# Performance work log

Hardware: AMD Instinct MI355X
Metric: run time of the kernel (lower is better)

The kernel has to match this reference:

```python
import jax, jax.numpy as jnp
import numpy as np

DIM = 1024
B, SQ, SK = 8, 2048, 2048


def setup_inputs() -> dict:
    key = jax.random.key(0)
    ks = jax.random.split(key, 8)
    s = 1.0 / np.sqrt(DIM)
    return {
        "x": jax.random.normal(ks[0], (B, SQ, DIM), dtype=jnp.float32),
        "context": jax.random.normal(ks[1], (B, SK, DIM), dtype=jnp.float32),
        "Wq": jax.random.normal(ks[2], (DIM, DIM), dtype=jnp.float32) * s,
        "bq": jnp.zeros((DIM,), dtype=jnp.float32),
        "Wk": jax.random.normal(ks[3], (DIM, DIM), dtype=jnp.float32) * s,
        "bk": jnp.zeros((DIM,), dtype=jnp.float32),
        "Wv": jax.random.normal(ks[4], (DIM, DIM), dtype=jnp.float32) * s,
        "bv": jnp.zeros((DIM,), dtype=jnp.float32),
    }


def reference(x, context, Wq, bq, Wk, bk, Wv, bv):
    # nn.Linear: y = x @ W.T + b
    q = jnp.einsum("bsd,ed->bse", x, Wq) + bq          # [B, SQ, D]
    k = jnp.einsum("btd,ed->bte", context, Wk) + bk    # [B, SK, D]
    v = jnp.einsum("btd,ed->bte", context, Wv) + bv    # [B, SK, D]
    scale = 1.0 / jnp.sqrt(jnp.asarray(x.shape[-1], dtype=x.dtype))
    scores = jnp.einsum("bse,bte->bst", q, k) * scale  # [B, SQ, SK]
    attn = jax.nn.softmax(scores, axis=-1)
    return jnp.einsum("bst,bte->bse", attn, v)         # [B, SQ, D]
```

## Files before the change

### kernel.cpp

```cpp
#include <hip/hip_runtime.h>
#include <hip/hip_bf16.h>
#include <hip/hip_fp16.h>

typedef float f32x4 __attribute__((ext_vector_type(4)));
typedef short short8 __attribute__((ext_vector_type(8)));
typedef _Float16 h4 __attribute__((ext_vector_type(4)));
typedef unsigned short u16;
typedef unsigned int u32;

#define LDK 40

__device__ __forceinline__ u16 bf16_rne(float x) {
  u32 u = __float_as_uint(x);
  u += 0x7FFFu + ((u >> 16) & 1u);
  return (u16)(u >> 16);
}
__device__ __forceinline__ u32 pack2(float a, float b) {
  return (u32)bf16_rne(a) | ((u32)bf16_rne(b) << 16);
}

__global__ __launch_bounds__(256)
void convert_kernel(const float* __restrict__ x, const float* __restrict__ ctx,
                    const float* __restrict__ wq, const float* __restrict__ wk,
                    const float* __restrict__ wv,
                    u16* __restrict__ xb, u16* __restrict__ cb,
                    u16* __restrict__ wqb, u16* __restrict__ wkb,
                    u16* __restrict__ wvb)
{
  int blk = blockIdx.x;
  const float* src; u16* dst; size_t off;
  if (blk < 8192)       { src = x;   dst = xb;  off = (size_t)blk * 2048; }
  else if (blk < 16384) { src = ctx; dst = cb;  off = (size_t)(blk - 8192) * 2048; }
  else if (blk < 16896) { src = wq;  dst = wqb; off = (size_t)(blk - 16384) * 2048; }
  else if (blk < 17408) { src = wk;  dst = wkb; off = (size_t)(blk - 16896) * 2048; }
  else                  { src = wv;  dst = wvb; off = (size_t)(blk - 17408) * 2048; }
  size_t e = off + (size_t)threadIdx.x * 8;
  float4 a = *(const float4*)(src + e);
  float4 b = *(const float4*)(src + e + 4);
  uint4 o;
  o.x = pack2(a.x, a.y); o.y = pack2(a.z, a.w);
  o.z = pack2(b.x, b.y); o.w = pack2(b.z, b.w);
  *(uint4*)(dst + e) = o;
}

__device__ __forceinline__ void stage_tile(const u16* __restrict__ G, int ld,
                                           int kt, u16* L, int tid) {
#pragma unroll
  for (int it = 0; it < 2; ++it) {
    int s = tid + 256 * it;
    int r = s >> 2, c = s & 3;
    *(uint4*)&L[r * LDK + c * 8] = *(const uint4*)(G + (size_t)r * ld + kt + c * 8);
  }
}

#define GEMM_FRAGS_AND_MFMA(Ah, Bh)                                            \
  short8 a_f[4], b_f[4];                                                       \
  _Pragma("unroll")                                                            \
  for (int i = 0; i < 4; ++i) {                                                \
    a_f[i] = *(const short8*)&Ah[(wm + i * 16 + lrow) * LDK + quad * 8];       \
    b_f[i] = *(const short8*)&Bh[(wn + i * 16 + lrow) * LDK + quad * 8];       \
  }                                                                            \
  _Pragma("unroll")                                                            \
  for (int i = 0; i < 4; ++i)                                                  \
    _Pragma("unroll")                                                          \
    for (int j = 0; j < 4; ++j)                                                \
      acc[i][j] = __builtin_amdgcn_mfma_f32_16x16x32_bf16(a_f[i], b_f[j], acc[i][j], 0, 0, 0);

#define GEMM_PROLOGUE                                                          \
  const int tid = threadIdx.x;                                                 \
  const int w = tid >> 6, lane = tid & 63;                                     \
  const int wm = (w >> 1) * 64, wn = (w & 1) * 64;                             \
  const int lrow = lane & 15, quad = lane >> 4;                                \
  f32x4 acc[4][4];                                                             \
  _Pragma("unroll")                                                            \
  for (int i = 0; i < 4; ++i)                                                  \
    _Pragma("unroll")                                                          \
    for (int j = 0; j < 4; ++j) {                                              \
      f32x4 z = {0.f, 0.f, 0.f, 0.f};                                          \
      acc[i][j] = z;                                                           \
    }

__global__ __launch_bounds__(256)
void projq_kernel(const u16* __restrict__ A, const u16* __restrict__ W,
                  const float* __restrict__ bias, u16* __restrict__ Y)
{
  __shared__ __align__(16) u16 Ah[128 * LDK];
  __shared__ __align__(16) u16 Bh[128 * LDK];
  const int m0 = blockIdx.y * 128, n0 = blockIdx.x * 128;
  GEMM_PROLOGUE
  const u16* A_b = A + (size_t)m0 * 1024;
  const u16* B_b = W + (size_t)n0 * 1024;

  for (int kt = 0; kt < 1024; kt += 32) {
    __syncthreads();
    stage_tile(A_b, 1024, kt, Ah, tid);
    stage_tile(B_b, 1024, kt, Bh, tid);
    __syncthreads();
    GEMM_FRAGS_AND_MFMA(Ah, Bh)
  }

#pragma unroll
  for (int j = 0; j < 4; ++j) {
    int gn = n0 + wn + j * 16 + lrow;
    float bj = bias[gn];
#pragma unroll
    for (int i = 0; i < 4; ++i) {
      int gm_base = m0 + wm + i * 16 + quad * 4;
#pragma unroll
      for (int r = 0; r < 4; ++r)
        Y[(size_t)(gm_base + r) * 1024 + gn] = bf16_rne(acc[i][j][r] + bj);
    }
  }
}

__global__ __launch_bounds__(256)
void projv_kernel(const u16* __restrict__ A, const u16* __restrict__ W,
                  const float* __restrict__ bias, u16* __restrict__ Vt)
{
  __shared__ __align__(16) u16 smem[128 * 136];
  u16* Ah = smem;
  u16* Bh = smem + 128 * LDK;
  const int m0 = blockIdx.y * 128, n0 = blockIdx.x * 128;
  const int bb = m0 >> 11, t0 = m0 & 2047;
  GEMM_PROLOGUE
  const u16* A_b = A + (size_t)m0 * 1024;
  const u16* B_b = W + (size_t)n0 * 1024;

  for (int kt = 0; kt < 1024; kt += 32) {
    __syncthreads();
    stage_tile(A_b, 1024, kt, Ah, tid);
    stage_tile(B_b, 1024, kt, Bh, tid);
    __syncthreads();
    GEMM_FRAGS_AND_MFMA(Ah, Bh)
  }

  __syncthreads();
  u16* T = smem;
#pragma unroll
  for (int j = 0; j < 4; ++j) {
    int e_l = wn + j * 16 + lrow;
    float bj = bias[n0 + e_l];
#pragma unroll
    for (int i = 0; i < 4; ++i) {
      int t_l = wm + i * 16 + quad * 4;
      uint2 p;
      p.x = pack2(acc[i][j][0] + bj, acc[i][j][1] + bj);
      p.y = pack2(acc[i][j][2] + bj, acc[i][j][3] + bj);
      *(uint2*)&T[e_l * 136 + t_l] = p;
    }
  }
  __syncthreads();

  int e_l = tid >> 1, half = tid & 1;
  u16* gdst = Vt + ((size_t)(bb * 1024 + n0 + e_l)) * 2048 + t0 + half * 64;
  const u16* Trow = &T[e_l * 136 + half * 64];
#pragma unroll
  for (int k = 0; k < 8; ++k)
    *(uint4*)(gdst + k * 8) = *(const uint4*)(Trow + k * 8);
}

__global__ __launch_bounds__(256)
void score_kernel(const u16* __restrict__ qb, const u16* __restrict__ kb,
                  _Float16* __restrict__ S)
{
  __shared__ __align__(16) u16 Ah[128 * LDK];
  __shared__ __align__(16) u16 Bh[128 * LDK];
  const int b = blockIdx.z;
  const int m0 = blockIdx.y * 128, n0 = blockIdx.x * 128;
  GEMM_PROLOGUE
  const u16* A_b = qb + ((size_t)b * 2048 + m0) * 1024;
  const u16* B_b = kb + ((size_t)b * 2048 + n0) * 1024;

  for (int kt = 0; kt < 1024; kt += 32) {
    __syncthreads();
    stage_tile(A_b, 1024, kt, Ah, tid);
    stage_tile(B_b, 1024, kt, Bh, tid);
    __syncthreads();
    GEMM_FRAGS_AND_MFMA(Ah, Bh)
  }

  const float scale = 0.03125f;
#pragma unroll
  for (int j = 0; j < 4; ++j) {
    int gn = n0 + wn + j * 16 + lrow;
#pragma unroll
    for (int i = 0; i < 4; ++i) {
      int gm_base = m0 + wm + i * 16 + quad * 4;
#pragma unroll
      for (int r = 0; r < 4; ++r)
        S[((size_t)b * 2048 + gm_base + r) * 2048 + gn] = (_Float16)(acc[i][j][r] * scale);
    }
  }
}

__global__ __launch_bounds__(256)
void softmax_kernel(_Float16* __restrict__ S)
{
  const int row = blockIdx.x;
  const int tid = threadIdx.x;
  _Float16* Sr = S + (size_t)row * 2048;
  h4 ah = *(const h4*)(Sr + tid * 4);
  h4 bh = *(const h4*)(Sr + 1024 + tid * 4);
  float a0 = (float)ah.x, a1 = (float)ah.y, a2 = (float)ah.z, a3 = (float)ah.w;
  float b0 = (float)bh.x, b1 = (float)bh.y, b2 = (float)bh.z, b3 = (float)bh.w;

  float m = fmaxf(fmaxf(fmaxf(a0, a1), fmaxf(a2, a3)),
                  fmaxf(fmaxf(b0, b1), fmaxf(b2, b3)));
#pragma unroll
  for (int off = 32; off > 0; off >>= 1) m = fmaxf(m, __shfl_xor(m, off));

  __shared__ float red[4];
  const int wid = tid >> 6, lane = tid & 63;
  if (lane == 0) red[wid] = m;
  __syncthreads();
  m = fmaxf(fmaxf(red[0], red[1]), fmaxf(red[2], red[3]));

  float e0 = __expf(a0 - m), e1 = __expf(a1 - m), e2 = __expf(a2 - m), e3 = __expf(a3 - m);
  float e4 = __expf(b0 - m), e5 = __expf(b1 - m), e6 = __expf(b2 - m), e7 = __expf(b3 - m);
  float s = ((e0 + e1) + (e2 + e3)) + ((e4 + e5) + (e6 + e7));
#pragma unroll
  for (int off = 32; off > 0; off >>= 1) s += __shfl_xor(s, off);
  __syncthreads();
  if (lane == 0) red[wid] = s;
  __syncthreads();
  s = red[0] + red[1] + red[2] + red[3];
  float inv = 1.0f / s;

  u16* P = (u16*)S;
  size_t pb = (size_t)row * 2048;
  uint2 w0, w1;
  w0.x = pack2(e0 * inv, e1 * inv);
  w0.y = pack2(e2 * inv, e3 * inv);
  w1.x = pack2(e4 * inv, e5 * inv);
  w1.y = pack2(e6 * inv, e7 * inv);
  *(uint2*)&P[pb + tid * 4] = w0;
  *(uint2*)&P[pb + 1024 + tid * 4] = w1;
}

__global__ __launch_bounds__(256)
void pv_kernel(const u16* __restrict__ P, const u16* __restrict__ Vt,
               float* __restrict__ O)
{
  __shared__ __align__(16) u16 Ah[128 * LDK];
  __shared__ __align__(16) u16 Bh[128 * LDK];
  const int b = blockIdx.z;
  const int m0 = blockIdx.y * 128, n0 = blockIdx.x * 128;
  GEMM_PROLOGUE
  const u16* A_b = P + ((size_t)b * 2048 + m0) * 2048;
  const u16* B_b = Vt + ((size_t)b * 1024 + n0) * 2048;

  for (int kt = 0; kt < 2048; kt += 32) {
    __syncthreads();
    stage_tile(A_b, 2048, kt, Ah, tid);
    stage_tile(B_b, 2048, kt, Bh, tid);
    __syncthreads();
    GEMM_FRAGS_AND_MFMA(Ah, Bh)
  }

#pragma unroll
  for (int j = 0; j < 4; ++j) {
    int gn = n0 + wn + j * 16 + lrow;
#pragma unroll
    for (int i = 0; i < 4; ++i) {
      int gm_base = m0 + wm + i * 16 + quad * 4;
#pragma unroll
      for (int r = 0; r < 4; ++r)
        O[((size_t)b * 2048 + gm_base + r) * 1024 + gn] = acc[i][j][r];
    }
  }
}

extern "C" void kernel_launch(void* const* d_in, const int* in_sizes, int n_in,
                              void* d_out, int out_size, void* d_ws, size_t ws_size,
                              hipStream_t stream) {
  const float* x   = (const float*)d_in[0];
  const float* ctx = (const float*)d_in[1];
  const float* Wq  = (const float*)d_in[2];
  const float* bq  = (const float*)d_in[3];
  const float* Wk  = (const float*)d_in[4];
  const float* bk  = (const float*)d_in[5];
  const float* Wv  = (const float*)d_in[6];
  const float* bv  = (const float*)d_in[7];
  float* out = (float*)d_out;

  const size_t NQ = (size_t)16384 * 1024;
  const size_t NW = (size_t)1024 * 1024;
  const size_t needed = (5 * NQ + 3 * NW) * sizeof(u16);
  if (ws_size < needed) return;

  u16* xb  = (u16*)d_ws;
  u16* cb  = xb + NQ;
  u16* qb  = cb + NQ;
  u16* kb  = qb + NQ;
  u16* vt  = kb + NQ;
  u16* wqb = vt + NQ;
  u16* wkb = wqb + NW;
  u16* wvb = wkb + NW;
  _Float16* S = (_Float16*)d_ws;

  dim3 blk(256, 1, 1);
  hipLaunchKernelGGL(convert_kernel, dim3(17920, 1, 1), blk, 0, stream,
                     x, ctx, Wq, Wk, Wv, xb, cb, wqb, wkb, wvb);
  hipLaunchKernelGGL(projq_kernel, dim3(8, 128, 1), blk, 0, stream, xb, wqb, bq, qb);
  hipLaunchKernelGGL(projq_kernel, dim3(8, 128, 1), blk, 0, stream, cb, wkb, bk, kb);
  hipLaunchKernelGGL(projv_kernel, dim3(8, 128, 1), blk, 0, stream, cb, wvb, bv, vt);
  hipLaunchKernelGGL(score_kernel, dim3(16, 16, 8), blk, 0, stream, qb, kb, S);
  hipLaunchKernelGGL(softmax_kernel, dim3(16384, 1, 1), blk, 0, stream, S);
  hipLaunchKernelGGL(pv_kernel, dim3(8, 16, 8), blk, 0, stream, (const u16*)S, vt, out);
}
```

Before: 599.2 us.

## Fuse fp32-to-bf16 activation conversion into projections and add XCD-aware block swizzle

The separate pass that converted x and context to bf16 is removed. The projection GEMMs now read the fp32 activations directly and pack them to bf16 while staging tiles, which saves a full write and re-read of the converted activations at the cost of twice the bytes per A-tile load. All GEMMs also remap block indices so that consecutive tiles land on the same XCD in groups of four rows, to improve L2 reuse. The softmax is changed to use a single 8-wide vector load and store per thread, and the score buffer moves to its own workspace region.

```diff
diff --git a/kernel.cpp b/kernel.cpp
--- a/kernel.cpp
+++ b/kernel.cpp
@@ -4,7 +4,6 @@
 
 typedef float f32x4 __attribute__((ext_vector_type(4)));
 typedef short short8 __attribute__((ext_vector_type(8)));
-typedef _Float16 h4 __attribute__((ext_vector_type(4)));
 typedef unsigned short u16;
 typedef unsigned int u32;
 
@@ -19,21 +18,31 @@
   return (u32)bf16_rne(a) | ((u32)bf16_rne(b) << 16);
 }
 
-__global__ __launch_bounds__(256)
-void convert_kernel(const float* __restrict__ x, const float* __restrict__ ctx,
-                    const float* __restrict__ wq, const float* __restrict__ wk,
-                    const float* __restrict__ wv,
-                    u16* __restrict__ xb, u16* __restrict__ cb,
-                    u16* __restrict__ wqb, u16* __restrict__ wkb,
-                    u16* __restrict__ wvb)
+__device__ __forceinline__ void swizzle_xcd(int gx, int gy, int& n, int& m, int& b) {
+  int lin = blockIdx.x + gx * (blockIdx.y + gy * blockIdx.z);
+  int total = gx * gy * (int)gridDim.z;
+  int chunk = total >> 3;
+  int nid = (lin & 7) * chunk + (lin >> 3);
+  int per_b = gx * gy;
+  b = nid / per_b;
+  int r = nid - b * per_b;
+  int grp = r / (gx * 4);
+  int q = r - grp * (gx * 4);
+  m = grp * 4 + (q & 3);
+  n = q >> 2;
+}
+
+__global__ __launch_bounds__(256)
+void convertw_kernel(const float* __restrict__ wq, const float* __restrict__ wk,
+                     const float* __restrict__ wv,
+                     u16* __restrict__ wqb, u16* __restrict__ wkb,
+                     u16* __restrict__ wvb)
 {
   int blk = blockIdx.x;
   const float* src; u16* dst; size_t off;
-  if (blk < 8192)       { src = x;   dst = xb;  off = (size_t)blk * 2048; }
-  else if (blk < 16384) { src = ctx; dst = cb;  off = (size_t)(blk - 8192) * 2048; }
-  else if (blk < 16896) { src = wq;  dst = wqb; off = (size_t)(blk - 16384) * 2048; }
-  else if (blk < 17408) { src = wk;  dst = wkb; off = (size_t)(blk - 16896) * 2048; }
-  else                  { src = wv;  dst = wvb; off = (size_t)(blk - 17408) * 2048; }
+  if (blk < 512)       { src = wq; dst = wqb; off = (size_t)blk * 2048; }
+  else if (blk < 1024) { src = wk; dst = wkb; off = (size_t)(blk - 512) * 2048; }
+  else                 { src = wv; dst = wvb; off = (size_t)(blk - 1024) * 2048; }
   size_t e = off + (size_t)threadIdx.x * 8;
   float4 a = *(const float4*)(src + e);
   float4 b = *(const float4*)(src + e + 4);
@@ -50,6 +59,22 @@
     int s = tid + 256 * it;
     int r = s >> 2, c = s & 3;
     *(uint4*)&L[r * LDK + c * 8] = *(const uint4*)(G + (size_t)r * ld + kt + c * 8);
+  }
+}
+
+__device__ __forceinline__ void stage_tile_f32(const float* __restrict__ G, int ld,
+                                               int kt, u16* L, int tid) {
+#pragma unroll
+  for (int it = 0; it < 2; ++it) {
+    int s = tid + 256 * it;
+    int r = s >> 2, c = s & 3;
+    const float* src = G + (size_t)r * ld + kt + c * 8;
+    float4 a = *(const float4*)src;
+    float4 b = *(const float4*)(src + 4);
+    uint4 o;
+    o.x = pack2(a.x, a.y); o.y = pack2(a.z, a.w);
+    o.z = pack2(b.x, b.y); o.w = pack2(b.z, b.w);
+    *(uint4*)&L[r * LDK + c * 8] = o;
   }
 }
 
@@ -81,19 +106,21 @@
     }
 
 __global__ __launch_bounds__(256)
-void projq_kernel(const u16* __restrict__ A, const u16* __restrict__ W,
+void projq_kernel(const float* __restrict__ A, const u16* __restrict__ W,
                   const float* __restrict__ bias, u16* __restrict__ Y)
 {
   __shared__ __align__(16) u16 Ah[128 * LDK];
   __shared__ __align__(16) u16 Bh[128 * LDK];
-  const int m0 = blockIdx.y * 128, n0 = blockIdx.x * 128;
+  int nt, mt, bz;
+  swizzle_xcd(gridDim.x, gridDim.y, nt, mt, bz);
+  const int m0 = mt * 128, n0 = nt * 128;
   GEMM_PROLOGUE
-  const u16* A_b = A + (size_t)m0 * 1024;
+  const float* A_b = A + (size_t)m0 * 1024;
   const u16* B_b = W + (size_t)n0 * 1024;
 
   for (int kt = 0; kt < 1024; kt += 32) {
     __syncthreads();
-    stage_tile(A_b, 1024, kt, Ah, tid);
+    stage_tile_f32(A_b, 1024, kt, Ah, tid);
     stage_tile(B_b, 1024, kt, Bh, tid);
     __syncthreads();
     GEMM_FRAGS_AND_MFMA(Ah, Bh)
@@ -114,21 +141,23 @@
 }
 
 __global__ __launch_bounds__(256)
-void projv_kernel(const u16* __restrict__ A, const u16* __restrict__ W,
+void projv_kernel(const float* __restrict__ A, const u16* __restrict__ W,
                   const float* __restrict__ bias, u16* __restrict__ Vt)
 {
   __shared__ __align__(16) u16 smem[128 * 136];
   u16* Ah = smem;
   u16* Bh = smem + 128 * LDK;
-  const int m0 = blockIdx.y * 128, n0 = blockIdx.x * 128;
+  int nt, mt, bz;
+  swizzle_xcd(gridDim.x, gridDim.y, nt, mt, bz);
+  const int m0 = mt * 128, n0 = nt * 128;
   const int bb = m0 >> 11, t0 = m0 & 2047;
   GEMM_PROLOGUE
-  const u16* A_b = A + (size_t)m0 * 1024;
+  const float* A_b = A + (size_t)m0 * 1024;
   const u16* B_b = W + (size_t)n0 * 1024;
 
   for (int kt = 0; kt < 1024; kt += 32) {
     __syncthreads();
-    stage_tile(A_b, 1024, kt, Ah, tid);
+    stage_tile_f32(A_b, 1024, kt, Ah, tid);
     stage_tile(B_b, 1024, kt, Bh, tid);
     __syncthreads();
     GEMM_FRAGS_AND_MFMA(Ah, Bh)
@@ -165,8 +194,9 @@
 {
   __shared__ __align__(16) u16 Ah[128 * LDK];
   __shared__ __align__(16) u16 Bh[128 * LDK];
-  const int b = blockIdx.z;
-  const int m0 = blockIdx.y * 128, n0 = blockIdx.x * 128;
+  int nt, mt, b;
+  swizzle_xcd(gridDim.x, gridDim.y, nt, mt, b);
+  const int m0 = mt * 128, n0 = nt * 128;
   GEMM_PROLOGUE
   const u16* A_b = qb + ((size_t)b * 2048 + m0) * 1024;
   const u16* B_b = kb + ((size_t)b * 2048 + n0) * 1024;
@@ -199,13 +229,15 @@
   const int row = blockIdx.x;
   const int tid = threadIdx.x;
   _Float16* Sr = S + (size_t)row * 2048;
-  h4 ah = *(const h4*)(Sr + tid * 4);
-  h4 bh = *(const h4*)(Sr + 1024 + tid * 4);
-  float a0 = (float)ah.x, a1 = (float)ah.y, a2 = (float)ah.z, a3 = (float)ah.w;
-  float b0 = (float)bh.x, b1 = (float)bh.y, b2 = (float)bh.z, b3 = (float)bh.w;
-
-  float m = fmaxf(fmaxf(fmaxf(a0, a1), fmaxf(a2, a3)),
-                  fmaxf(fmaxf(b0, b1), fmaxf(b2, b3)));
+  typedef _Float16 h8 __attribute__((ext_vector_type(8)));
+  h8 v = *(const h8*)(Sr + tid * 8);
+  float f[8];
+#pragma unroll
+  for (int i = 0; i < 8; ++i) f[i] = (float)v[i];
+
+  float m = f[0];
+#pragma unroll
+  for (int i = 1; i < 8; ++i) m = fmaxf(m, f[i]);
 #pragma unroll
   for (int off = 32; off > 0; off >>= 1) m = fmaxf(m, __shfl_xor(m, off));
 
@@ -215,9 +247,9 @@
   __syncthreads();
   m = fmaxf(fmaxf(red[0], red[1]), fmaxf(red[2], red[3]));
 
-  float e0 = __expf(a0 - m), e1 = __expf(a1 - m), e2 = __expf(a2 - m), e3 = __expf(a3 - m);
-  float e4 = __expf(b0 - m), e5 = __expf(b1 - m), e6 = __expf(b2 - m), e7 = __expf(b3 - m);
-  float s = ((e0 + e1) + (e2 + e3)) + ((e4 + e5) + (e6 + e7));
+  float e[8], s = 0.f;
+#pragma unroll
+  for (int i = 0; i < 8; ++i) { e[i] = __expf(f[i] - m); s += e[i]; }
 #pragma unroll
   for (int off = 32; off > 0; off >>= 1) s += __shfl_xor(s, off);
   __syncthreads();
@@ -227,14 +259,12 @@
   float inv = 1.0f / s;
 
   u16* P = (u16*)S;
-  size_t pb = (size_t)row * 2048;
-  uint2 w0, w1;
-  w0.x = pack2(e0 * inv, e1 * inv);
-  w0.y = pack2(e2 * inv, e3 * inv);
-  w1.x = pack2(e4 * inv, e5 * inv);
-  w1.y = pack2(e6 * inv, e7 * inv);
-  *(uint2*)&P[pb + tid * 4] = w0;
-  *(uint2*)&P[pb + 1024 + tid * 4] = w1;
+  uint4 o;
+  o.x = pack2(e[0] * inv, e[1] * inv);
+  o.y = pack2(e[2] * inv, e[3] * inv);
+  o.z = pack2(e[4] * inv, e[5] * inv);
+  o.w = pack2(e[6] * inv, e[7] * inv);
+  *(uint4*)&P[(size_t)row * 2048 + tid * 8] = o;
 }
 
 __global__ __launch_bounds__(256)
@@ -243,8 +273,9 @@
 {
   __shared__ __align__(16) u16 Ah[128 * LDK];
   __shared__ __align__(16) u16 Bh[128 * LDK];
-  const int b = blockIdx.z;
-  const int m0 = blockIdx.y * 128, n0 = blockIdx.x * 128;
+  int nt, mt, b;
+  swizzle_xcd(gridDim.x, gridDim.y, nt, mt, b);
+  const int m0 = mt * 128, n0 = nt * 128;
   GEMM_PROLOGUE
   const u16* A_b = P + ((size_t)b * 2048 + m0) * 2048;
   const u16* B_b = Vt + ((size_t)b * 1024 + n0) * 2048;
@@ -285,25 +316,24 @@
 
   const size_t NQ = (size_t)16384 * 1024;
   const size_t NW = (size_t)1024 * 1024;
-  const size_t needed = (5 * NQ + 3 * NW) * sizeof(u16);
+  const size_t needed = (3 * NQ + 3 * NW) * sizeof(u16)
+                      + (size_t)16384 * 2048 * sizeof(_Float16);
   if (ws_size < needed) return;
 
-  u16* xb  = (u16*)d_ws;
-  u16* cb  = xb + NQ;
-  u16* qb  = cb + NQ;
+  u16* qb  = (u16*)d_ws;
   u16* kb  = qb + NQ;
   u16* vt  = kb + NQ;
   u16* wqb = vt + NQ;
   u16* wkb = wqb + NW;
   u16* wvb = wkb + NW;
-  _Float16* S = (_Float16*)d_ws;
+  _Float16* S = (_Float16*)(wvb + NW);
 
   dim3 blk(256, 1, 1);
-  hipLaunchKernelGGL(convert_kernel, dim3(17920, 1, 1), blk, 0, stream,
-                     x, ctx, Wq, Wk, Wv, xb, cb, wqb, wkb, wvb);
-  hipLaunchKernelGGL(projq_kernel, dim3(8, 128, 1), blk, 0, stream, xb, wqb, bq, qb);
-  hipLaunchKernelGGL(projq_kernel, dim3(8, 128, 1), blk, 0, stream, cb, wkb, bk, kb);
-  hipLaunchKernelGGL(projv_kernel, dim3(8, 128, 1), blk, 0, stream, cb, wvb, bv, vt);
+  hipLaunchKernelGGL(convertw_kernel, dim3(1536, 1, 1), blk, 0, stream,
+                     Wq, Wk, Wv, wqb, wkb, wvb);
+  hipLaunchKernelGGL(projq_kernel, dim3(8, 128, 1), blk, 0, stream, x,   wqb, bq, qb);
+  hipLaunchKernelGGL(projq_kernel, dim3(8, 128, 1), blk, 0, stream, ctx, wkb, bk, kb);
+  hipLaunchKernelGGL(projv_kernel, dim3(8, 128, 1), blk, 0, stream, ctx, wvb, bv, vt);
   hipLaunchKernelGGL(score_kernel, dim3(16, 16, 8), blk, 0, stream, qb, kb, S);
   hipLaunchKernelGGL(softmax_kernel, dim3(16384, 1, 1), blk, 0, stream, S);
   hipLaunchKernelGGL(pv_kernel, dim3(8, 16, 8), blk, 0, stream, (const u16*)S, vt, out);
```

New measurement: 625.3 us. 1.04x slower.
